# Performance work log

Hardware: AMD Instinct MI355X
Metric: run time of the kernel (lower is better)

Reference implementation:

```python
import jax, jax.numpy as jnp
import numpy as np

M, N, NNZ, NITER = 1_000_000, 1_000_000, 8_000_000, 5


def setup_inputs() -> dict:
    key = jax.random.key(0)
    ks = jax.random.split(key, 24)
    f32 = jnp.float32
    inp = dict(
        rows=jax.random.randint(ks[0], (NNZ,), 0, M, dtype=jnp.int32),
        cols=jax.random.randint(ks[1], (NNZ,), 0, N, dtype=jnp.int32),
        vals=jax.random.normal(ks[2], (NNZ,), dtype=f32) * 0.1,
        b=jax.random.normal(ks[3], (M, 1), dtype=f32),
        c=jax.random.normal(ks[4], (N, 1), dtype=f32),
        solution=jax.random.normal(ks[5], (N, 1), dtype=f32),
        dual_solution=jax.random.normal(ks[6], (M, 1), dtype=f32),
        x0=jax.random.normal(ks[7], (N, 1), dtype=f32),  # beta=1 init
        y0=jax.random.normal(ks[8], (M, 1), dtype=f32),  # std_y=1 init
        # dual tower: Conv1d(10->4), Conv1d(6->4), update Conv1d(6->1)
        dw1=jax.random.normal(ks[9], (4, 10), dtype=f32) * 0.3,
        db1=jax.random.normal(ks[10], (4,), dtype=f32) * 0.1,
        dw2=jax.random.normal(ks[11], (4, 6), dtype=f32) * 0.3,
        db2=jax.random.normal(ks[12], (4,), dtype=f32) * 0.1,
        dwu=jax.random.normal(ks[13], (1, 6), dtype=f32) * 0.1,
        dbu=jax.random.normal(ks[14], (1,), dtype=f32) * 0.1,
        # primal tower: Conv1d(10->4), Conv1d(6->4), update Conv1d(6->1)
        pw1=jax.random.normal(ks[15], (4, 10), dtype=f32) * 0.3,
        pb1=jax.random.normal(ks[16], (4,), dtype=f32) * 0.1,
        pw2=jax.random.normal(ks[17], (4, 6), dtype=f32) * 0.3,
        pb2=jax.random.normal(ks[18], (4,), dtype=f32) * 0.1,
        pwu=jax.random.normal(ks[19], (1, 6), dtype=f32) * 0.1,
        pbu=jax.random.normal(ks[20], (1,), dtype=f32) * 0.1,
        nb_max_iter=NITER,
    )
    return inp


def reference(rows, cols, vals, b, c, solution, dual_solution, x0, y0,
              dw1, db1, dw2, db2, dwu, dbu,
              pw1, pb1, pw2, pb2, pwu, pbu, nb_max_iter):
    m, n = b.shape[0], c.shape[0]

    def A_mm(X):   # sparse A @ X : [n,k] -> [m,k]
        return jax.ops.segment_sum(vals[:, None] * X[cols], rows, num_segments=m)

    def At_mm(Y):  # sparse A.T @ Y : [m,k] -> [n,k]
        return jax.ops.segment_sum(vals[:, None] * Y[rows], cols, num_segments=n)

    def step(carry, _):
        x, y, x_h, y_h = carry  # x[n,1] y[m,1] x_h[4,n] y_h[4,m]
        # dual update
        r = A_mm(x) - b                                   # [m,1]
        atxh = A_mm(x_h.T)                                # [m,4]
        h = jnp.concatenate([y_h, atxh.T, y.T, r.T], 0)   # [10,m]
        h = jax.nn.relu(dw1 @ h + db1[:, None])           # [4,m]
        h = jnp.concatenate([h, y.T, r.T], 0)             # [6,m]
        y_h = jax.nn.relu(dw2 @ h + db2[:, None])         # [4,m]
        h2 = jnp.concatenate([y_h, y.T, r.T], 0)          # [6,m]
        y = y + (dwu @ h2 + dbu[:, None]).T               # [m,1]
        # primal update
        d = c + At_mm(y)                                  # [n,1]
        atyh = At_mm(y_h.T)                               # [n,4]
        g = jnp.concatenate([x_h, atyh.T, x.T, d.T], 0)   # [10,n]
        g = jax.nn.relu(pw1 @ g + pb1[:, None])           # [4,n]
        g = jnp.concatenate([g, x.T, d.T], 0)             # [6,n]
        x_h = jax.nn.relu(pw2 @ g + pb2[:, None])         # [4,n]
        g2 = jnp.concatenate([x_h, x.T, d.T], 0)          # [6,n]
        x = x + (pwu @ g2 + pbu[:, None]).T               # [n,1]
        dp = jnp.sqrt(jnp.sum((x - solution) ** 2))
        dd = jnp.sqrt(jnp.sum((y - dual_solution) ** 2))
        return (x, y, x_h, y_h), (dp, dd)

    init = (x0, y0,
            jnp.zeros((4, n), dtype=x0.dtype),
            jnp.zeros((4, m), dtype=y0.dtype))
    (x, y, _, _), (dps, dds) = jax.lax.scan(step, init, None, length=nb_max_iter)

    loss_primal = jnp.mean(dps) + 1.0 * jnp.mean(jax.nn.relu(dps[1:] - dps[:-1]))
    loss_dual = jnp.mean(dds) + 1.0 * jnp.mean(jax.nn.relu(dds[1:] - dds[:-1]))
    loss = loss_primal + loss_dual
    return x, y, loss, dps, dds
```

## Files before the change

kernel.cpp:

```cpp
#include <hip/hip_runtime.h>
#include <math.h>


#define NITER 5
#define NBK_SHIFT 9
#define NBK (1 << NBK_SHIFT)
#define NBK_MAX 2048
#define CH 32768
#define SORT_CAP 6144

__device__ __forceinline__ float blockReduceSum(float v) {
#pragma unroll
  for (int off = 32; off > 0; off >>= 1) v += __shfl_down(v, off, 64);
  __shared__ float smem[8];
  const int lane = threadIdx.x & 63;
  const int wid = threadIdx.x >> 6;
  if (lane == 0) smem[wid] = v;
  __syncthreads();
  float r = 0.f;
  if (threadIdx.x == 0) {
    const int nw = (blockDim.x + 63) >> 6;
    for (int w = 0; w < nw; ++w) r += smem[w];
  }
  return r;
}

__global__ __launch_bounds__(1024) void zero_meta(int* __restrict__ cntA,
                                                  int* __restrict__ cntT,
                                                  float* __restrict__ red) {
  const int i = threadIdx.x;
  cntA[i] = 0;
  cntA[i + 1024] = 0;
  cntT[i] = 0;
  cntT[i + 1024] = 0;
  if (i < 16) red[i] = 0.f;
}

__global__ __launch_bounds__(256) void hist2(const int* __restrict__ rows,
                                             const int* __restrict__ cols,
                                             int* __restrict__ cntA,
                                             int* __restrict__ cntT, int nnz) {
  __shared__ int hA[NBK_MAX];
  __shared__ int hT[NBK_MAX];
  for (int i = threadIdx.x; i < NBK_MAX; i += 256) { hA[i] = 0; hT[i] = 0; }
  __syncthreads();
  const int stride = gridDim.x * blockDim.x;
  for (int e = blockIdx.x * blockDim.x + threadIdx.x; e < nnz; e += stride) {
    atomicAdd(&hA[rows[e] >> NBK_SHIFT], 1);
    atomicAdd(&hT[cols[e] >> NBK_SHIFT], 1);
  }
  __syncthreads();
  for (int i = threadIdx.x; i < NBK_MAX; i += 256) {
    if (hA[i]) atomicAdd(&cntA[i], hA[i]);
    if (hT[i]) atomicAdd(&cntT[i], hT[i]);
  }
}

__global__ __launch_bounds__(1024) void scan_bases(const int* __restrict__ cnt,
                                                   int* __restrict__ base,
                                                   int* __restrict__ fill,
                                                   int nb) {
  __shared__ int sm[1024];
  int run = 0;
  for (int s = 0; s < nb; s += 1024) {
    const int i = s + threadIdx.x;
    const int x = (i < nb) ? cnt[i] : 0;
    sm[threadIdx.x] = x;
    __syncthreads();
#pragma unroll
    for (int off = 1; off < 1024; off <<= 1) {
      const int add = (threadIdx.x >= off) ? sm[threadIdx.x - off] : 0;
      __syncthreads();
      sm[threadIdx.x] += add;
      __syncthreads();
    }
    if (i < nb) {
      const int ex = run + sm[threadIdx.x] - x;
      base[i] = ex;
      fill[i] = ex;
    }
    const int tot = sm[1023];
    __syncthreads();
    run += tot;
  }
}

__global__ __launch_bounds__(512) void scatter2(
    const int* __restrict__ rows, const int* __restrict__ cols,
    const float* __restrict__ vals, int* __restrict__ fillA,
    int* __restrict__ fillT, int2* __restrict__ eA, int2* __restrict__ eT,
    int nnz) {
  __shared__ int hA[NBK_MAX];
  __shared__ int hT[NBK_MAX];
  for (int i = threadIdx.x; i < NBK_MAX; i += 512) { hA[i] = 0; hT[i] = 0; }
  __syncthreads();
  const int e0 = blockIdx.x * CH;
  for (int k = threadIdx.x; k < CH; k += 512) {
    const int e = e0 + k;
    if (e < nnz) {
      atomicAdd(&hA[rows[e] >> NBK_SHIFT], 1);
      atomicAdd(&hT[cols[e] >> NBK_SHIFT], 1);
    }
  }
  __syncthreads();
  for (int i = threadIdx.x; i < NBK_MAX; i += 512) {
    const int cA = hA[i];
    if (cA) hA[i] = atomicAdd(&fillA[i], cA);
    const int cT = hT[i];
    if (cT) hT[i] = atomicAdd(&fillT[i], cT);
  }
  __syncthreads();
  for (int k = threadIdx.x; k < CH; k += 512) {
    const int e = e0 + k;
    if (e < nnz) {
      const int r = rows[e];
      const int c = cols[e];
      const int vb = __float_as_int(vals[e]);
      const int pA = atomicAdd(&hA[r >> NBK_SHIFT], 1);
      eA[pA] = make_int2(((r & (NBK - 1)) << 20) | c, vb);
      const int pT = atomicAdd(&hT[c >> NBK_SHIFT], 1);
      eT[pT] = make_int2(((c & (NBK - 1)) << 20) | r, vb);
    }
  }
}

__global__ __launch_bounds__(256) void sort_bucket(const int* __restrict__ base,
                                                   const int* __restrict__ cnt,
                                                   int2* __restrict__ edges) {
  __shared__ int2 recs[SORT_CAP];
  __shared__ int hist[NBK];
  __shared__ int wsum[256];
  const int bkt = blockIdx.x;
  const int beg = base[bkt];
  const int num = cnt[bkt];
  if (num > SORT_CAP) return;
  for (int i = threadIdx.x; i < NBK; i += 256) hist[i] = 0;
  __syncthreads();
  for (int k = threadIdx.x; k < num; k += 256) {
    const int2 r = edges[beg + k];
    recs[k] = r;
    atomicAdd(&hist[((unsigned)r.x) >> 20], 1);
  }
  __syncthreads();
  const int b2 = threadIdx.x * 2;
  const int h0 = hist[b2];
  const int h1 = hist[b2 + 1];
  wsum[threadIdx.x] = h0 + h1;
  __syncthreads();
#pragma unroll
  for (int off = 1; off < 256; off <<= 1) {
    const int add = (threadIdx.x >= off) ? wsum[threadIdx.x - off] : 0;
    __syncthreads();
    wsum[threadIdx.x] += add;
    __syncthreads();
  }
  const int excl = (threadIdx.x == 0) ? 0 : wsum[threadIdx.x - 1];
  __syncthreads();
  hist[b2] = excl;
  hist[b2 + 1] = excl + h0;
  __syncthreads();
  for (int k = threadIdx.x; k < num; k += 256) {
    const int2 r = recs[k];
    const int p = atomicAdd(&hist[((unsigned)r.x) >> 20], 1);
    edges[beg + p] = r;
  }
}

__global__ __launch_bounds__(256) void init_state2(const float* __restrict__ x0,
                                                   const float* __restrict__ y0,
                                                   float* __restrict__ X5,
                                                   float* __restrict__ Y5,
                                                   int n, int m) {
  const int i = blockIdx.x * blockDim.x + threadIdx.x;
  if (i < n) {
    float* xp = X5 + (size_t)i * 8;
    xp[0] = x0[i];
    xp[1] = 0.f; xp[2] = 0.f; xp[3] = 0.f; xp[4] = 0.f;
  }
  if (i < m) {
    float* yp = Y5 + (size_t)i * 8;
    yp[0] = y0[i];
    yp[1] = 0.f; yp[2] = 0.f; yp[3] = 0.f; yp[4] = 0.f;
  }
}

__global__ __launch_bounds__(256) void fused_bucket_tower(
    const int* __restrict__ base, const int* __restrict__ cnt,
    const int2* __restrict__ edges, const float* __restrict__ src,
    float* __restrict__ state, const float* __restrict__ seed, float sign,
    const float* __restrict__ sol, const float* __restrict__ w1,
    const float* __restrict__ b1, const float* __restrict__ w2,
    const float* __restrict__ b2, const float* __restrict__ wu,
    const float* __restrict__ bu, float* __restrict__ red_slot, int count) {
  __shared__ float acc[NBK * 5];
  for (int i = threadIdx.x; i < NBK * 5; i += 256) acc[i] = 0.f;
  __syncthreads();
  const int bkt = blockIdx.x;
  const int beg = base[bkt];
  const int num = cnt[bkt];
  const int lane = threadIdx.x & 63;
  for (int k0 = 0; k0 < num; k0 += 256) {
    const int k = k0 + threadIdx.x;
    int dl = -1;
    float m0 = 0.f, m1 = 0.f, m2 = 0.f, m3 = 0.f, m4 = 0.f;
    if (k < num) {
      const int2 ed = edges[beg + k];
      dl = ((unsigned)ed.x) >> 20;
      const int sc = ed.x & 0xFFFFF;
      const float v = __int_as_float(ed.y);
      const float* sp = src + (size_t)sc * 8;
      const float4 lo = *reinterpret_cast<const float4*>(sp);
      m0 = v * lo.x; m1 = v * lo.y; m2 = v * lo.z; m3 = v * lo.w;
      m4 = v * sp[4];
    }
#pragma unroll
    for (int off = 1; off < 64; off <<= 1) {
      const int dlu = __shfl_up(dl, off, 64);
      const float t0 = __shfl_up(m0, off, 64);
      const float t1 = __shfl_up(m1, off, 64);
      const float t2 = __shfl_up(m2, off, 64);
      const float t3 = __shfl_up(m3, off, 64);
      const float t4 = __shfl_up(m4, off, 64);
      if (lane >= off && dlu == dl) {
        m0 += t0; m1 += t1; m2 += t2; m3 += t3; m4 += t4;
      }
    }
    const int dld = __shfl_down(dl, 1, 64);
    const bool last = (lane == 63) || (dld != dl);
    if (dl >= 0 && last) {
      float* ap = acc + dl * 5;
      atomicAdd(ap + 0, m0);
      atomicAdd(ap + 1, m1);
      atomicAdd(ap + 2, m2);
      atomicAdd(ap + 3, m3);
      atomicAdd(ap + 4, m4);
    }
  }
  __syncthreads();
  float part = 0.f;
  for (int t = threadIdx.x; t < NBK; t += 256) {
    const int row = (bkt << NBK_SHIFT) + t;
    if (row < count) {
      const float* a = acc + t * 5;
      const float r = a[0] + sign * seed[row];
      float* sp = state + (size_t)row * 8;
      const float4 st = *reinterpret_cast<const float4*>(sp);
      const float y = st.x;
      float v[10];
      v[0] = st.y; v[1] = st.z; v[2] = st.w; v[3] = sp[4];
      v[4] = a[1]; v[5] = a[2]; v[6] = a[3]; v[7] = a[4];
      v[8] = y;
      v[9] = r;
      float h[4];
#pragma unroll
      for (int o = 0; o < 4; ++o) {
        float accv = b1[o];
#pragma unroll
        for (int kk = 0; kk < 10; ++kk) accv += w1[o * 10 + kk] * v[kk];
        h[o] = fmaxf(accv, 0.f);
      }
      float hn[4];
#pragma unroll
      for (int o = 0; o < 4; ++o) {
        float accv = b2[o] + w2[o * 6 + 4] * y + w2[o * 6 + 5] * r;
#pragma unroll
        for (int kk = 0; kk < 4; ++kk) accv += w2[o * 6 + kk] * h[kk];
        hn[o] = fmaxf(accv, 0.f);
      }
      const float upd = bu[0] + wu[0] * hn[0] + wu[1] * hn[1] + wu[2] * hn[2] +
                        wu[3] * hn[3] + wu[4] * y + wu[5] * r;
      const float yn = y + upd;
      float4 stn;
      stn.x = yn; stn.y = hn[0]; stn.z = hn[1]; stn.w = hn[2];
      *reinterpret_cast<float4*>(sp) = stn;
      sp[4] = hn[3];
      const float diff = yn - sol[row];
      part += diff * diff;
    }
  }
  const float bs = blockReduceSum(part);
  if (threadIdx.x == 0) unsafeAtomicAdd(red_slot, bs);
}

__global__ __launch_bounds__(256) void finalize2(const float* __restrict__ X5,
                                                 const float* __restrict__ Y5,
                                                 const float* __restrict__ red,
                                                 float* __restrict__ out, int n,
                                                 int m) {
  const int i = blockIdx.x * blockDim.x + threadIdx.x;
  if (i < n) out[i] = X5[(size_t)i * 8];
  if (i < m) out[n + i] = Y5[(size_t)i * 8];
  if (i == 0) {
    float dps[NITER], dds[NITER];
#pragma unroll
    for (int t = 0; t < NITER; ++t) {
      dps[t] = sqrtf(red[t]);
      dds[t] = sqrtf(red[NITER + t]);
    }
    float mp = 0.f, md = 0.f, rp = 0.f, rd = 0.f;
#pragma unroll
    for (int t = 0; t < NITER; ++t) { mp += dps[t]; md += dds[t]; }
#pragma unroll
    for (int t = 1; t < NITER; ++t) {
      rp += fmaxf(dps[t] - dps[t - 1], 0.f);
      rd += fmaxf(dds[t] - dds[t - 1], 0.f);
    }
    out[n + m] = mp / NITER + rp / (NITER - 1) + md / NITER + rd / (NITER - 1);
#pragma unroll
    for (int t = 0; t < NITER; ++t) {
      out[n + m + 1 + t] = dps[t];
      out[n + m + 1 + NITER + t] = dds[t];
    }
  }
}

template <int S>
__global__ __launch_bounds__(256) void init_state(
    const float* __restrict__ x0, const float* __restrict__ y0,
    const float* __restrict__ b, float* __restrict__ X5,
    float* __restrict__ Y5, float* __restrict__ Yacc, float* __restrict__ red,
    int n, int m) {
  const int i = blockIdx.x * blockDim.x + threadIdx.x;
  if (i < 16) red[i] = 0.f;
  if (i < n) {
    float* xp = X5 + (size_t)i * S;
    xp[0] = x0[i];
    xp[1] = 0.f; xp[2] = 0.f; xp[3] = 0.f; xp[4] = 0.f;
  }
  if (i < m) {
    float* yp = Y5 + (size_t)i * S;
    yp[0] = y0[i];
    yp[1] = 0.f; yp[2] = 0.f; yp[3] = 0.f; yp[4] = 0.f;
    float* ya = Yacc + (size_t)i * S;
    ya[0] = -b[i];
    ya[1] = 0.f; ya[2] = 0.f; ya[3] = 0.f; ya[4] = 0.f;
  }
}

template <int S>
__global__ __launch_bounds__(256) void spmm5(const int* __restrict__ gidx,
                                             const int* __restrict__ sidx,
                                             const float* __restrict__ vals,
                                             const float* __restrict__ src,
                                             float* __restrict__ dst, int nnz) {
  const int e = blockIdx.x * blockDim.x + threadIdx.x;
  if (e >= nnz) return;
  const int g = gidx[e];
  const int s = sidx[e];
  const float v = vals[e];
  const float* sp = src + (size_t)g * S;
  float s0, s1, s2, s3, s4;
  if constexpr (S == 8) {
    const float4 lo = *reinterpret_cast<const float4*>(sp);
    s0 = lo.x; s1 = lo.y; s2 = lo.z; s3 = lo.w; s4 = sp[4];
  } else {
    s0 = sp[0]; s1 = sp[1]; s2 = sp[2]; s3 = sp[3]; s4 = sp[4];
  }
  float* dp = dst + (size_t)s * S;
  unsafeAtomicAdd(dp + 0, v * s0);
  unsafeAtomicAdd(dp + 1, v * s1);
  unsafeAtomicAdd(dp + 2, v * s2);
  unsafeAtomicAdd(dp + 3, v * s3);
  unsafeAtomicAdd(dp + 4, v * s4);
}

template <int S>
__global__ __launch_bounds__(256) void tower(
    const float* __restrict__ acc, float* __restrict__ state,
    const float* __restrict__ prep_src, float* __restrict__ prep_dst,
    float sign, const float* __restrict__ sol, const float* __restrict__ w1,
    const float* __restrict__ b1, const float* __restrict__ w2,
    const float* __restrict__ b2, const float* __restrict__ wu,
    const float* __restrict__ bu, float* __restrict__ red_slot, int count,
    int prep_count) {
  const int i = blockIdx.x * blockDim.x + threadIdx.x;
  float part = 0.f;
  if (i < count) {
    const float* a = acc + (size_t)i * S;
    const float r = a[0];
    float* sp = state + (size_t)i * S;
    const float y = sp[0];
    float v[10];
    v[0] = sp[1]; v[1] = sp[2]; v[2] = sp[3]; v[3] = sp[4];
    v[4] = a[1];  v[5] = a[2];  v[6] = a[3];  v[7] = a[4];
    v[8] = y;
    v[9] = r;
    float h[4];
#pragma unroll
    for (int o = 0; o < 4; ++o) {
      float accv = b1[o];
#pragma unroll
      for (int k = 0; k < 10; ++k) accv += w1[o * 10 + k] * v[k];
      h[o] = fmaxf(accv, 0.f);
    }
    float hn[4];
#pragma unroll
    for (int o = 0; o < 4; ++o) {
      float accv = b2[o] + w2[o * 6 + 4] * y + w2[o * 6 + 5] * r;
#pragma unroll
      for (int k = 0; k < 4; ++k) accv += w2[o * 6 + k] * h[k];
      hn[o] = fmaxf(accv, 0.f);
    }
    const float upd = bu[0] + wu[0] * hn[0] + wu[1] * hn[1] + wu[2] * hn[2] +
                      wu[3] * hn[3] + wu[4] * y + wu[5] * r;
    const float yn = y + upd;
    sp[0] = yn;
    sp[1] = hn[0]; sp[2] = hn[1]; sp[3] = hn[2]; sp[4] = hn[3];
    const float diff = yn - sol[i];
    part = diff * diff;
  }
  if (i < prep_count) {
    float* pd = prep_dst + (size_t)i * S;
    pd[0] = sign * prep_src[i];
    pd[1] = 0.f; pd[2] = 0.f; pd[3] = 0.f; pd[4] = 0.f;
  }
  const float bs = blockReduceSum(part);
  if (threadIdx.x == 0) unsafeAtomicAdd(red_slot, bs);
}

template <int S>
static void run_atomic(const int* rows, const int* cols, const float* vals,
                       const float* b, const float* c, const float* solution,
                       const float* dual_solution, const float* x0,
                       const float* y0, const float* dw1, const float* db1,
                       const float* dw2, const float* db2, const float* dwu,
                       const float* dbu, const float* pw1, const float* pb1,
                       const float* pw2, const float* pb2, const float* pwu,
                       const float* pbu, float* out, float* ws, int n, int m,
                       int nnz, hipStream_t stream) {
  float* X5 = ws;
  float* Y5 = X5 + (size_t)n * S;
  float* Xacc = Y5 + (size_t)m * S;
  float* Yacc = Xacc + (size_t)n * S;
  float* red = Yacc + (size_t)m * S;

  const int BLK = 256;
  const int nm = (n > m) ? n : m;
  const int gN = (nm + BLK - 1) / BLK;
  const int gE = (nnz + BLK - 1) / BLK;

  init_state<S><<<gN, BLK, 0, stream>>>(x0, y0, b, X5, Y5, Yacc, red, n, m);
  for (int t = 0; t < NITER; ++t) {
    spmm5<S><<<gE, BLK, 0, stream>>>(cols, rows, vals, X5, Yacc, nnz);
    tower<S><<<gN, BLK, 0, stream>>>(Yacc, Y5, c, Xacc, 1.0f, dual_solution,
                                     dw1, db1, dw2, db2, dwu, dbu,
                                     red + NITER + t, m, n);
    spmm5<S><<<gE, BLK, 0, stream>>>(rows, cols, vals, Y5, Xacc, nnz);
    tower<S><<<gN, BLK, 0, stream>>>(Xacc, X5, b, Yacc, -1.0f, solution, pw1,
                                     pb1, pw2, pb2, pwu, pbu, red + t, n, m);
  }
  finalize2<<<gN, BLK, 0, stream>>>(X5, Y5, red, out, n, m);
}

static inline size_t alignUp(size_t x, size_t a) { return (x + a - 1) / a * a; }

extern "C" void kernel_launch(void* const* d_in, const int* in_sizes, int n_in,
                              void* d_out, int out_size, void* d_ws,
                              size_t ws_size, hipStream_t stream) {
  const int* rows = (const int*)d_in[0];
  const int* cols = (const int*)d_in[1];
  const float* vals = (const float*)d_in[2];
  const float* b = (const float*)d_in[3];
  const float* c = (const float*)d_in[4];
  const float* solution = (const float*)d_in[5];
  const float* dual_solution = (const float*)d_in[6];
  const float* x0 = (const float*)d_in[7];
  const float* y0 = (const float*)d_in[8];
  const float* dw1 = (const float*)d_in[9];
  const float* db1 = (const float*)d_in[10];
  const float* dw2 = (const float*)d_in[11];
  const float* db2 = (const float*)d_in[12];
  const float* dwu = (const float*)d_in[13];
  const float* dbu = (const float*)d_in[14];
  const float* pw1 = (const float*)d_in[15];
  const float* pb1 = (const float*)d_in[16];
  const float* pw2 = (const float*)d_in[17];
  const float* pb2 = (const float*)d_in[18];
  const float* pwu = (const float*)d_in[19];
  const float* pbu = (const float*)d_in[20];

  const int nnz = in_sizes[0];
  const int m = in_sizes[3];
  const int n = in_sizes[4];
  float* out = (float*)d_out;
  char* ws = (char*)d_ws;

  const int nbA = (m + NBK - 1) >> NBK_SHIFT;
  const int nbT = (n + NBK - 1) >> NBK_SHIFT;

  size_t off = 0;
  const size_t oX5 = off;    off = alignUp(off + (size_t)n * 8 * 4, 256);
  const size_t oY5 = off;    off = alignUp(off + (size_t)m * 8 * 4, 256);
  const size_t oEA = off;    off = alignUp(off + (size_t)nnz * 8, 256);
  const size_t oET = off;    off = alignUp(off + (size_t)nnz * 8, 256);
  const size_t oCntA = off;  off = alignUp(off + (size_t)NBK_MAX * 4, 256);
  const size_t oBasA = off;  off = alignUp(off + (size_t)NBK_MAX * 4, 256);
  const size_t oFilA = off;  off = alignUp(off + (size_t)NBK_MAX * 4, 256);
  const size_t oCntT = off;  off = alignUp(off + (size_t)NBK_MAX * 4, 256);
  const size_t oBasT = off;  off = alignUp(off + (size_t)NBK_MAX * 4, 256);
  const size_t oFilT = off;  off = alignUp(off + (size_t)NBK_MAX * 4, 256);
  const size_t oRed = off;   off = alignUp(off + 16 * 4, 256);
  const size_t needB = off;

  const bool ok = (nbA <= NBK_MAX) && (nbT <= NBK_MAX) && (m <= (1 << 20)) &&
                  (n <= (1 << 20)) && (ws_size >= needB);

  if (ok) {
    float* X5 = (float*)(ws + oX5);
    float* Y5 = (float*)(ws + oY5);
    int2* eA = (int2*)(ws + oEA);
    int2* eT = (int2*)(ws + oET);
    int* cntA = (int*)(ws + oCntA);
    int* basA = (int*)(ws + oBasA);
    int* filA = (int*)(ws + oFilA);
    int* cntT = (int*)(ws + oCntT);
    int* basT = (int*)(ws + oBasT);
    int* filT = (int*)(ws + oFilT);
    float* red = (float*)(ws + oRed);

    const int BLK = 256;
    const int nm = (n > m) ? n : m;
    const int gN = (nm + BLK - 1) / BLK;
    const int gC = (nnz + CH - 1) / CH;

    zero_meta<<<1, 1024, 0, stream>>>(cntA, cntT, red);
    hist2<<<256, BLK, 0, stream>>>(rows, cols, cntA, cntT, nnz);
    scan_bases<<<1, 1024, 0, stream>>>(cntA, basA, filA, nbA);
    scan_bases<<<1, 1024, 0, stream>>>(cntT, basT, filT, nbT);
    scatter2<<<gC, 512, 0, stream>>>(rows, cols, vals, filA, filT, eA, eT,
                                     nnz);
    sort_bucket<<<nbA, BLK, 0, stream>>>(basA, cntA, eA);
    sort_bucket<<<nbT, BLK, 0, stream>>>(basT, cntT, eT);
    init_state2<<<gN, BLK, 0, stream>>>(x0, y0, X5, Y5, n, m);

    for (int t = 0; t < NITER; ++t) {
      fused_bucket_tower<<<nbA, BLK, 0, stream>>>(
          basA, cntA, eA, X5, Y5, b, -1.0f, dual_solution, dw1, db1, dw2, db2,
          dwu, dbu, red + NITER + t, m);
      fused_bucket_tower<<<nbT, BLK, 0, stream>>>(
          basT, cntT, eT, Y5, X5, c, 1.0f, solution, pw1, pb1, pw2, pb2, pwu,
          pbu, red + t, n);
    }
    finalize2<<<gN, BLK, 0, stream>>>(X5, Y5, red, out, n, m);
    return;
  }

  const size_t need8 =
      ((size_t)n * 8 + (size_t)m * 8) * 2 * sizeof(float) + 64 * sizeof(float);
  if (ws_size >= need8) {
    run_atomic<8>(rows, cols, vals, b, c, solution, dual_solution, x0, y0, dw1,
                  db1, dw2, db2, dwu, dbu, pw1, pb1, pw2, pb2, pwu, pbu, out,
                  (float*)d_ws, n, m, nnz, stream);
  } else {
    run_atomic<5>(rows, cols, vals, b, c, solution, dual_solution, x0, y0, dw1,
                  db1, dw2, db2, dwu, dbu, pw1, pb1, pw2, pb2, pwu, pbu, out,
                  (float*)d_ws, n, m, nnz, stream);
  }
}
```

Baseline: 2.311 ms.

## Widen sort blocks, halve scatter chunks, and batch two edges per gather loop

```diff
diff --git a/kernel.cpp b/kernel.cpp
--- a/kernel.cpp
+++ b/kernel.cpp
@@ -6,7 +6,7 @@
 #define NBK_SHIFT 9
 #define NBK (1 << NBK_SHIFT)
 #define NBK_MAX 2048
-#define CH 32768
+#define CH 16384
 #define SORT_CAP 6144
 
 __device__ __forceinline__ float blockReduceSum(float v) {
@@ -124,42 +124,39 @@
   }
 }
 
-__global__ __launch_bounds__(256) void sort_bucket(const int* __restrict__ base,
+__global__ __launch_bounds__(512) void sort_bucket(const int* __restrict__ base,
                                                    const int* __restrict__ cnt,
                                                    int2* __restrict__ edges) {
   __shared__ int2 recs[SORT_CAP];
   __shared__ int hist[NBK];
-  __shared__ int wsum[256];
   const int bkt = blockIdx.x;
   const int beg = base[bkt];
   const int num = cnt[bkt];
   if (num > SORT_CAP) return;
-  for (int i = threadIdx.x; i < NBK; i += 256) hist[i] = 0;
-  __syncthreads();
-  for (int k = threadIdx.x; k < num; k += 256) {
+  if (threadIdx.x < NBK) hist[threadIdx.x] = 0;
+  __syncthreads();
+  for (int k = threadIdx.x; k < num; k += 512) {
     const int2 r = edges[beg + k];
     recs[k] = r;
     atomicAdd(&hist[((unsigned)r.x) >> 20], 1);
   }
   __syncthreads();
-  const int b2 = threadIdx.x * 2;
-  const int h0 = hist[b2];
-  const int h1 = hist[b2 + 1];
-  wsum[threadIdx.x] = h0 + h1;
-  __syncthreads();
-#pragma unroll
-  for (int off = 1; off < 256; off <<= 1) {
-    const int add = (threadIdx.x >= off) ? wsum[threadIdx.x - off] : 0;
+  int x = 0, incl = 0;
+  if (threadIdx.x < NBK) { x = hist[threadIdx.x]; incl = x; }
+#pragma unroll
+  for (int off = 1; off < NBK; off <<= 1) {
+    int add = 0;
+    if (threadIdx.x < NBK && threadIdx.x >= off) add = hist[threadIdx.x - off];
     __syncthreads();
-    wsum[threadIdx.x] += add;
+    if (threadIdx.x < NBK) {
+      incl += add;
+      hist[threadIdx.x] = incl;
+    }
     __syncthreads();
   }
-  const int excl = (threadIdx.x == 0) ? 0 : wsum[threadIdx.x - 1];
-  __syncthreads();
-  hist[b2] = excl;
-  hist[b2 + 1] = excl + h0;
-  __syncthreads();
-  for (int k = threadIdx.x; k < num; k += 256) {
+  if (threadIdx.x < NBK) hist[threadIdx.x] = incl - x;
+  __syncthreads();
+  for (int k = threadIdx.x; k < num; k += 512) {
     const int2 r = recs[k];
     const int p = atomicAdd(&hist[((unsigned)r.x) >> 20], 1);
     edges[beg + p] = r;
@@ -199,41 +196,81 @@
   const int beg = base[bkt];
   const int num = cnt[bkt];
   const int lane = threadIdx.x & 63;
-  for (int k0 = 0; k0 < num; k0 += 256) {
-    const int k = k0 + threadIdx.x;
-    int dl = -1;
-    float m0 = 0.f, m1 = 0.f, m2 = 0.f, m3 = 0.f, m4 = 0.f;
-    if (k < num) {
-      const int2 ed = edges[beg + k];
-      dl = ((unsigned)ed.x) >> 20;
-      const int sc = ed.x & 0xFFFFF;
-      const float v = __int_as_float(ed.y);
-      const float* sp = src + (size_t)sc * 8;
-      const float4 lo = *reinterpret_cast<const float4*>(sp);
-      m0 = v * lo.x; m1 = v * lo.y; m2 = v * lo.z; m3 = v * lo.w;
-      m4 = v * sp[4];
-    }
-#pragma unroll
-    for (int off = 1; off < 64; off <<= 1) {
-      const int dlu = __shfl_up(dl, off, 64);
-      const float t0 = __shfl_up(m0, off, 64);
-      const float t1 = __shfl_up(m1, off, 64);
-      const float t2 = __shfl_up(m2, off, 64);
-      const float t3 = __shfl_up(m3, off, 64);
-      const float t4 = __shfl_up(m4, off, 64);
-      if (lane >= off && dlu == dl) {
-        m0 += t0; m1 += t1; m2 += t2; m3 += t3; m4 += t4;
+  for (int k0 = 0; k0 < num; k0 += 512) {
+    const int kA = k0 + threadIdx.x;
+    const int kB = k0 + 256 + threadIdx.x;
+    int dlA = -1, dlB = -1;
+    float vA = 0.f, vB = 0.f;
+    float4 loA = make_float4(0.f, 0.f, 0.f, 0.f);
+    float4 loB = make_float4(0.f, 0.f, 0.f, 0.f);
+    float s4A = 0.f, s4B = 0.f;
+    if (kA < num) {
+      const int2 ed = edges[beg + kA];
+      dlA = ((unsigned)ed.x) >> 20;
+      vA = __int_as_float(ed.y);
+      const float* sp = src + (size_t)(ed.x & 0xFFFFF) * 8;
+      loA = *reinterpret_cast<const float4*>(sp);
+      s4A = sp[4];
+    }
+    if (kB < num) {
+      const int2 ed = edges[beg + kB];
+      dlB = ((unsigned)ed.x) >> 20;
+      vB = __int_as_float(ed.y);
+      const float* sp = src + (size_t)(ed.x & 0xFFFFF) * 8;
+      loB = *reinterpret_cast<const float4*>(sp);
+      s4B = sp[4];
+    }
+    {
+      float m0 = vA * loA.x, m1 = vA * loA.y, m2 = vA * loA.z,
+            m3 = vA * loA.w, m4 = vA * s4A;
+      int dl = dlA;
+#pragma unroll
+      for (int off = 1; off < 64; off <<= 1) {
+        const int dlu = __shfl_up(dl, off, 64);
+        const float t0 = __shfl_up(m0, off, 64);
+        const float t1 = __shfl_up(m1, off, 64);
+        const float t2 = __shfl_up(m2, off, 64);
+        const float t3 = __shfl_up(m3, off, 64);
+        const float t4 = __shfl_up(m4, off, 64);
+        if (lane >= off && dlu == dl) {
+          m0 += t0; m1 += t1; m2 += t2; m3 += t3; m4 += t4;
+        }
       }
-    }
-    const int dld = __shfl_down(dl, 1, 64);
-    const bool last = (lane == 63) || (dld != dl);
-    if (dl >= 0 && last) {
-      float* ap = acc + dl * 5;
-      atomicAdd(ap + 0, m0);
-      atomicAdd(ap + 1, m1);
-      atomicAdd(ap + 2, m2);
-      atomicAdd(ap + 3, m3);
-      atomicAdd(ap + 4, m4);
+      const int dld = __shfl_down(dl, 1, 64);
+      if (dl >= 0 && ((lane == 63) || (dld != dl))) {
+        float* ap = acc + dl * 5;
+        atomicAdd(ap + 0, m0);
+        atomicAdd(ap + 1, m1);
+        atomicAdd(ap + 2, m2);
+        atomicAdd(ap + 3, m3);
+        atomicAdd(ap + 4, m4);
+      }
+    }
+    {
+      float m0 = vB * loB.x, m1 = vB * loB.y, m2 = vB * loB.z,
+            m3 = vB * loB.w, m4 = vB * s4B;
+      int dl = dlB;
+#pragma unroll
+      for (int off = 1; off < 64; off <<= 1) {
+        const int dlu = __shfl_up(dl, off, 64);
+        const float t0 = __shfl_up(m0, off, 64);
+        const float t1 = __shfl_up(m1, off, 64);
+        const float t2 = __shfl_up(m2, off, 64);
+        const float t3 = __shfl_up(m3, off, 64);
+        const float t4 = __shfl_up(m4, off, 64);
+        if (lane >= off && dlu == dl) {
+          m0 += t0; m1 += t1; m2 += t2; m3 += t3; m4 += t4;
+        }
+      }
+      const int dld = __shfl_down(dl, 1, 64);
+      if (dl >= 0 && ((lane == 63) || (dld != dl))) {
+        float* ap = acc + dl * 5;
+        atomicAdd(ap + 0, m0);
+        atomicAdd(ap + 1, m1);
+        atomicAdd(ap + 2, m2);
+        atomicAdd(ap + 3, m3);
+        atomicAdd(ap + 4, m4);
+      }
     }
   }
   __syncthreads();
@@ -524,13 +561,13 @@
     const int gC = (nnz + CH - 1) / CH;
 
     zero_meta<<<1, 1024, 0, stream>>>(cntA, cntT, red);
-    hist2<<<256, BLK, 0, stream>>>(rows, cols, cntA, cntT, nnz);
+    hist2<<<512, BLK, 0, stream>>>(rows, cols, cntA, cntT, nnz);
     scan_bases<<<1, 1024, 0, stream>>>(cntA, basA, filA, nbA);
     scan_bases<<<1, 1024, 0, stream>>>(cntT, basT, filT, nbT);
     scatter2<<<gC, 512, 0, stream>>>(rows, cols, vals, filA, filT, eA, eT,
                                      nnz);
-    sort_bucket<<<nbA, BLK, 0, stream>>>(basA, cntA, eA);
-    sort_bucket<<<nbT, BLK, 0, stream>>>(basT, cntT, eT);
+    sort_bucket<<<nbA, 512, 0, stream>>>(basA, cntA, eA);
+    sort_bucket<<<nbT, 512, 0, stream>>>(basT, cntT, eT);
     init_state2<<<gN, BLK, 0, stream>>>(x0, y0, X5, Y5, n, m);
 
     for (int t = 0; t < NITER; ++t) {
```

After: 2.267 ms. Within noise of the previous version (-1.9%).
